# Optimization experiments

Hardware: AMD Instinct MI355X
Metric: run time of the kernel (lower is better)

The kernel has to match this reference:

```python
import jax, jax.numpy as jnp
import numpy as np
from jax import lax

K, INC, OUC = 6, 64, 32
H, W = 512, 512
WIN = 128  # min(128, min(H,W)) for training path
ITERATION = 2  # torch uses random.randint(1,3); fixed for determinism


def setup_inputs() -> dict:
    key = jax.random.key(0)
    ks = jax.random.split(key, 12)
    s = 0.05
    return {
        "x": jax.random.uniform(ks[0], (K, 3, H, W), jnp.float32),
        "pred_list": jax.random.uniform(ks[1], (K, 3, H, W), jnp.float32),
        "feat_list": jax.random.normal(ks[2], (K, INC, H, W), jnp.float32) * 0.1,
        "split_w": jax.random.normal(ks[3], (3 * OUC, INC, 3, 3), jnp.float32) * s,
        "split_b": jax.random.normal(ks[4], (3 * OUC,), jnp.float32) * s,
        "merge1_w": jax.random.normal(ks[5], (INC, 3 * OUC + 3, 3, 3), jnp.float32) * s,
        "merge1_b": jax.random.normal(ks[6], (INC,), jnp.float32) * s,
        "merge2_w": jax.random.normal(ks[7], (INC, INC, 3, 3), jnp.float32) * s,
        "merge2_b": jax.random.normal(ks[8], (INC,), jnp.float32) * s,
        "head_w": jax.random.normal(ks[9], (3, INC, 3, 3), jnp.float32) * s,
        "head_b": jax.random.normal(ks[10], (3,), jnp.float32) * s,
    }


def _conv(x, w, b, groups=1):
    y = lax.conv_general_dilated(
        x, w, (1, 1), ((1, 1), (1, 1)),
        dimension_numbers=("NCHW", "OIHW", "NCHW"), feature_group_count=groups)
    return y + b[None, :, None, None]


def _get_box(pred_list):
    # B_cat = mean of bg channel, T_cat = sum of fg channel; distance map [H,W]
    B_cat = pred_list[:, 2].mean(axis=0)
    T_cat = pred_list[:, 0].sum(axis=0)
    distance = jnp.abs(1.0 - T_cat - B_cat)
    # nearest-neighbor downsample by 0.1: out[i,j] = in[10*i, 10*j]
    hs, ws = H // 10, W // 10
    ds = distance[::10, ::10][:hs, :ws]
    # NMS keep[0] (training path uses boxes[0:1]) == global argmax of score
    idx = jnp.argmax(ds.reshape(-1))
    cx = (idx % ws) * 10
    cy = (idx // ws) * 10
    half = WIN // 2
    x1, y1 = cx - half, cy - half
    x2, y2 = cx + half, cy + half
    ox = (-jnp.minimum(x1, 0) + jnp.minimum(W - x1, 0)
          - jnp.minimum(x2, 0) + jnp.minimum(W - x2, 0))
    oy = (-jnp.minimum(y1, 0) + jnp.minimum(H - y1, 0)
          - jnp.minimum(y2, 0) + jnp.minimum(H - y2, 0))
    return (y1 + oy).astype(jnp.int32), (x1 + ox).astype(jnp.int32)


def reference(x, pred_list, feat_list, split_w, split_b,
              merge1_w, merge1_b, merge2_w, merge2_b, head_w, head_b):
    c = INC
    y1, x1 = _get_box(pred_list)  # box fixed across iterations (computed once)
    x_patch = lax.dynamic_slice(x, (0, 0, y1, x1), (K, 3, WIN, WIN))
    feat_patch = lax.dynamic_slice(feat_list, (0, 0, y1, x1), (K, INC, WIN, WIN))
    feat_tiled = jnp.tile(feat_patch, (1, 3, 1, 1))
    denom = max(K - 1, 1)

    pl = pred_list
    for _ in range(ITERATION):
        pred_patch = lax.dynamic_slice(pl, (0, 0, y1, x1), (K, 3, WIN, WIN))
        # cat([p0.repeat(c), p1.repeat(c), p2.repeat(c)]) == repeat each channel c times
        attention = jnp.repeat(pred_patch, c, axis=1)
        fs = _conv(feat_tiled * attention, split_w, split_b, groups=3)
        f0, f1, f2 = fs[:, :OUC], fs[:, OUC:2 * OUC], fs[:, 2 * OUC:]
        feat_t = f1.sum(0, keepdims=True) / denom - f0.sum(0, keepdims=True) + 2.0 * f0
        feat_r = f0.sum(0, keepdims=True) - f0 + f1
        feat_b = jnp.broadcast_to(f2.mean(0, keepdims=True), f2.shape)
        fcat = jnp.concatenate([feat_t, feat_r, feat_b, x_patch], axis=1)
        h1 = jax.nn.leaky_relu(_conv(fcat, merge1_w, merge1_b), 0.2)
        fm = _conv(h1, merge2_w, merge2_b)
        pr = _conv(fm, head_w, head_b)
        inner = (jnp.tanh(pr[:, :, 10:WIN - 10, 10:WIN - 10]) + 1.0) / 2.0
        pl = lax.dynamic_update_slice(pl, inner, (0, 0, y1 + 10, x1 + 10))
    return pl
```

## Files before the change

### kernel.cpp

```cpp
#include <hip/hip_runtime.h>
#include <math.h>

typedef __attribute__((ext_vector_type(8))) short short8_t;
typedef __attribute__((ext_vector_type(4))) float f32x4;

#define Hh 512
#define Ww 512
#define IMG (Hh * Ww)
#define WINP 128
#define PP (WINP * WINP)

__device__ __forceinline__ unsigned short f2bf(float f) {
    unsigned int u = __builtin_bit_cast(unsigned int, f);
    u += 0x7fffu + ((u >> 16) & 1u);
    return (unsigned short)(u >> 16);
}
__device__ __forceinline__ float bf2f(unsigned short h) {
    unsigned int u = ((unsigned int)h) << 16;
    return __builtin_bit_cast(float, u);
}

__global__ void box_kernel(const float* __restrict__ pred, int* __restrict__ box) {
    int tid = threadIdx.x;
    float best = -1.0f; int bidx = 0x7fffffff;
    for (int cand = tid; cand < 51 * 51; cand += 256) {
        int i = cand / 51, j = cand % 51;
        int y = i * 10, x = j * 10;
        float T = 0.f, Bv = 0.f;
#pragma unroll
        for (int k = 0; k < 6; ++k) {
            T  += pred[((k * 3 + 0) * Hh + y) * Ww + x];
            Bv += pred[((k * 3 + 2) * Hh + y) * Ww + x];
        }
        float d = fabsf(1.0f - T - Bv / 6.0f);
        if (d > best || (d == best && cand < bidx)) { best = d; bidx = cand; }
    }
    __shared__ float sv[256];
    __shared__ int   si[256];
    sv[tid] = best; si[tid] = bidx;
    __syncthreads();
    for (int s = 128; s > 0; s >>= 1) {
        if (tid < s) {
            if (sv[tid + s] > sv[tid] || (sv[tid + s] == sv[tid] && si[tid + s] < si[tid])) {
                sv[tid] = sv[tid + s]; si[tid] = si[tid + s];
            }
        }
        __syncthreads();
    }
    if (tid == 0) {
        int idx = si[0];
        int cy = (idx / 51) * 10, cx = (idx % 51) * 10;
        int yy = cy - 64; yy = yy < 0 ? 0 : (yy > Hh - WINP ? Hh - WINP : yy);
        int xx = cx - 64; xx = xx < 0 ? 0 : (xx > Ww - WINP ? Ww - WINP : xx);
        box[0] = yy; box[1] = xx;
    }
}

__global__ void copy_kernel(const float4* __restrict__ src, float4* __restrict__ dst) {
    int i = blockIdx.x * 256 + threadIdx.x;
    dst[i] = src[i];
}

__global__ void prep_weights(const float* __restrict__ sw, const float* __restrict__ m1w,
                             const float* __restrict__ m2w, const float* __restrict__ hw,
                             unsigned short* __restrict__ WF)
{
    int idx = blockIdx.x * 256 + threadIdx.x;
    int j = idx & 7;
    int lane = (idx >> 3) & 63;
    int frag = idx >> 9;
    int n16 = lane & 15;
    int ko = (lane >> 4) * 8 + j;
    float v = 0.f;
    if (frag < 108) {
        int g = frag / 36; int r = frag % 36; int kc = r / 18; r %= 18; int tap = r / 2; int nf = r & 1;
        int oc = g * 32 + nf * 16 + n16; int ic = kc * 32 + ko;
        v = sw[(oc * 64 + ic) * 9 + tap];
    } else if (frag < 252) {
        int r = frag - 108; int half = r / 72; r %= 72; int kc = r / 18; r %= 18; int tap = r / 2; int nf = r & 1;
        int oc = half * 32 + nf * 16 + n16; int ic = kc * 32 + ko;
        if (ic < 99) v = m1w[(oc * 99 + ic) * 9 + tap];
    } else if (frag < 324) {
        int r = frag - 252; int half = r / 36; r %= 36; int kc = r / 18; r %= 18; int tap = r / 2; int nf = r & 1;
        int oc = half * 32 + nf * 16 + n16; int ic = kc * 32 + ko;
        v = m2w[(oc * 64 + ic) * 9 + tap];
    } else {
        int r = frag - 324; int kc = r / 9; int tap = r % 9;
        int ic = kc * 32 + ko;
        if (n16 < 3) v = hw[(n16 * 64 + ic) * 9 + tap];
    }
    WF[idx] = f2bf(v);
}

__global__ void prep_featcl(const float* __restrict__ feat, const int* __restrict__ box,
                            unsigned short* __restrict__ featcl)
{
    int row = blockIdx.x;
    int k = blockIdx.y;
    int t = threadIdx.x;
    int y1 = box[0], x1 = box[1];
    __shared__ unsigned short s[128 * 64];
    for (int i = 0; i < 32; ++i) {
        int idx = t + i * 256;
        int ic = idx >> 7, c = idx & 127;
        s[c * 64 + ic] = f2bf(feat[((size_t)(k * 64 + ic) * Hh + y1 + row) * Ww + x1 + c]);
    }
    __syncthreads();
    if (t < 128) {
        unsigned short* dst = &featcl[((size_t)k * 16384 + row * 128 + t) * 64];
        for (int i = 0; i < 8; ++i)
            *(short8_t*)&dst[i * 8] = *(short8_t*)&s[t * 64 + i * 8];
    }
}

__global__ __launch_bounds__(256) void split_mfma(
    const unsigned short* __restrict__ featcl, const float* __restrict__ pl,
    const unsigned short* __restrict__ WF, const float* __restrict__ sb,
    const int* __restrict__ box, unsigned short* __restrict__ fscl)
{
    const int tid = threadIdx.x;
    const int l = tid & 63, w = tid >> 6;
    const int T = blockIdx.x;
    const int k = blockIdx.y / 3, g = blockIdx.y % 3;
    const int ty0 = (T >> 3) * 16, tx0 = (T & 7) * 16;
    const int y1 = box[0], x1 = box[1];

    __shared__ __align__(16) unsigned short s_a[10368];
    __shared__ __align__(16) unsigned short s_b[9216];

    f32x4 acc[4][2];
#pragma unroll
    for (int mf = 0; mf < 4; ++mf)
#pragma unroll
        for (int nf = 0; nf < 2; ++nf) acc[mf][nf] = (f32x4){0.f, 0.f, 0.f, 0.f};

    const float* plg = pl + (size_t)(k * 3 + g) * IMG + (size_t)y1 * Ww + x1;
    const unsigned short* fck = featcl + (size_t)k * 16384 * 64;

    for (int kc = 0; kc < 2; ++kc) {
        __syncthreads();
#pragma unroll
        for (int i = 0; i < 6; ++i) {
            int s = tid + i * 256;
            if (s < 1296) {
                int pxs = s >> 2, q = s & 3;
                int r = pxs / 18, c = pxs - r * 18;
                int py = ty0 - 1 + r, px = tx0 - 1 + c;
                short8_t o;
                if (py >= 0 && py < WINP && px >= 0 && px < WINP) {
                    float pv = plg[py * Ww + px];
                    short8_t f = *(const short8_t*)&fck[(size_t)(py * WINP + px) * 64 + kc * 32 + q * 8];
#pragma unroll
                    for (int e = 0; e < 8; ++e) o[e] = (short)f2bf(bf2f((unsigned short)f[e]) * pv);
                } else {
#pragma unroll
                    for (int e = 0; e < 8; ++e) o[e] = 0;
                }
                *(short8_t*)&s_a[(r * 18 + c) * 32 + q * 8] = o;
            }
        }
        {
            const unsigned short* src = WF + (size_t)((g * 2 + kc) * 18) * 512;
#pragma unroll
            for (int i = 0; i < 5; ++i) {
                int cch = tid + i * 256;
                if (cch < 1152)
                    *(short8_t*)&s_b[cch * 8] = *(const short8_t*)&src[cch * 8];
            }
        }
        __syncthreads();
#pragma unroll
        for (int tap = 0; tap < 9; ++tap) {
            int dy = tap / 3, dx = tap % 3;
            short8_t a[4];
#pragma unroll
            for (int mf = 0; mf < 4; ++mf)
                a[mf] = *(const short8_t*)&s_a[((w * 4 + mf + dy) * 18 + (l & 15) + dx) * 32 + (l >> 4) * 8];
#pragma unroll
            for (int nf = 0; nf < 2; ++nf) {
                short8_t bfr = *(const short8_t*)&s_b[((tap * 2 + nf) * 64 + l) * 8];
#pragma unroll
                for (int mf = 0; mf < 4; ++mf)
                    acc[mf][nf] = __builtin_amdgcn_mfma_f32_16x16x32_bf16(a[mf], bfr, acc[mf][nf], 0, 0, 0);
            }
        }
    }
    __syncthreads();
    unsigned short* s_t = s_a;
#pragma unroll
    for (int nf = 0; nf < 2; ++nf) {
        float bias = sb[g * 32 + nf * 16 + (l & 15)];
#pragma unroll
        for (int mf = 0; mf < 4; ++mf) {
            int row = w * 4 + mf;
#pragma unroll
            for (int r = 0; r < 4; ++r) {
                int col = (l >> 4) * 4 + r;
                s_t[(row * 16 + col) * 32 + nf * 16 + (l & 15)] = f2bf(acc[mf][nf][r] + bias);
            }
        }
    }
    __syncthreads();
    {
        int row = tid >> 4, col = tid & 15;
        size_t gpx = (size_t)(ty0 + row) * WINP + tx0 + col;
        unsigned short* dst = fscl + ((size_t)k * 16384 + gpx) * 96 + g * 32;
#pragma unroll
        for (int i = 0; i < 4; ++i)
            *(short8_t*)&dst[i * 8] = *(short8_t*)&s_t[tid * 32 + i * 8];
    }
}

__global__ void reduce_kernel(const unsigned short* __restrict__ fscl, float* __restrict__ Scl)
{
    int tg = blockIdx.x * 256 + threadIdx.x;
    int px = tg >> 2, q = tg & 3;
    float s0[8], s1[8], s2[8];
#pragma unroll
    for (int e = 0; e < 8; ++e) { s0[e] = 0.f; s1[e] = 0.f; s2[e] = 0.f; }
#pragma unroll
    for (int k = 0; k < 6; ++k) {
        const unsigned short* p = &fscl[((size_t)k * 16384 + px) * 96 + q * 8];
        short8_t a0 = *(const short8_t*)&p[0];
        short8_t a1 = *(const short8_t*)&p[32];
        short8_t a2 = *(const short8_t*)&p[64];
#pragma unroll
        for (int e = 0; e < 8; ++e) {
            s0[e] += bf2f((unsigned short)a0[e]);
            s1[e] += bf2f((unsigned short)a1[e]);
            s2[e] += bf2f((unsigned short)a2[e]);
        }
    }
    float* d = &Scl[(size_t)px * 96 + q * 8];
#pragma unroll
    for (int e = 0; e < 8; ++e) {
        d[e]      = s1[e] * 0.2f - s0[e];
        d[32 + e] = s0[e];
        d[64 + e] = s2[e] * (1.f / 6.f);
    }
}

__global__ __launch_bounds__(256) void merge1_mfma(
    const unsigned short* __restrict__ fscl, const float* __restrict__ Scl,
    const float* __restrict__ x, const unsigned short* __restrict__ WF,
    const float* __restrict__ m1b, const int* __restrict__ box,
    unsigned short* __restrict__ h1cl)
{
    const int tid = threadIdx.x;
    const int l = tid & 63, w = tid >> 6;
    const int T = blockIdx.x;
    const int k = blockIdx.y >> 1, half = blockIdx.y & 1;
    const int ty0 = (T >> 3) * 16, tx0 = (T & 7) * 16;
    const int y1 = box[0], x1 = box[1];

    __shared__ __align__(16) unsigned short s_a[10368];
    __shared__ __align__(16) unsigned short s_b[9216];

    f32x4 acc[4][2];
#pragma unroll
    for (int mf = 0; mf < 4; ++mf)
#pragma unroll
        for (int nf = 0; nf < 2; ++nf) acc[mf][nf] = (f32x4){0.f, 0.f, 0.f, 0.f};

    for (int kc = 0; kc < 4; ++kc) {
        __syncthreads();
#pragma unroll
        for (int i = 0; i < 6; ++i) {
            int s = tid + i * 256;
            if (s < 1296) {
                int pxs = s >> 2, q = s & 3;
                int r = pxs / 18, c = pxs - r * 18;
                int py = ty0 - 1 + r, px = tx0 - 1 + c;
                short8_t o;
#pragma unroll
                for (int e = 0; e < 8; ++e) o[e] = 0;
                if (py >= 0 && py < WINP && px >= 0 && px < WINP) {
                    size_t gpx = (size_t)py * WINP + px;
                    if (kc == 0) {
                        short8_t f0 = *(const short8_t*)&fscl[((size_t)k * 16384 + gpx) * 96 + q * 8];
                        const float* S = &Scl[gpx * 96 + q * 8];
#pragma unroll
                        for (int e = 0; e < 8; ++e)
                            o[e] = (short)f2bf(S[e] + 2.f * bf2f((unsigned short)f0[e]));
                    } else if (kc == 1) {
                        const unsigned short* fp = &fscl[((size_t)k * 16384 + gpx) * 96];
                        short8_t f0 = *(const short8_t*)&fp[q * 8];
                        short8_t f1 = *(const short8_t*)&fp[32 + q * 8];
                        const float* S = &Scl[gpx * 96 + 32 + q * 8];
#pragma unroll
                        for (int e = 0; e < 8; ++e)
                            o[e] = (short)f2bf(S[e] - bf2f((unsigned short)f0[e]) + bf2f((unsigned short)f1[e]));
                    } else if (kc == 2) {
                        const float* S = &Scl[gpx * 96 + 64 + q * 8];
#pragma unroll
                        for (int e = 0; e < 8; ++e) o[e] = (short)f2bf(S[e]);
                    } else {
                        if (q == 0) {
#pragma unroll
                            for (int ch = 0; ch < 3; ++ch)
                                o[ch] = (short)f2bf(x[(size_t)(k * 3 + ch) * IMG + (size_t)(y1 + py) * Ww + x1 + px]);
                        }
                    }
                }
                *(short8_t*)&s_a[(r * 18 + c) * 32 + q * 8] = o;
            }
        }
        {
            const unsigned short* src = WF + (size_t)(108 + (half * 4 + kc) * 18) * 512;
#pragma unroll
            for (int i = 0; i < 5; ++i) {
                int cch = tid + i * 256;
                if (cch < 1152)
                    *(short8_t*)&s_b[cch * 8] = *(const short8_t*)&src[cch * 8];
            }
        }
        __syncthreads();
#pragma unroll
        for (int tap = 0; tap < 9; ++tap) {
            int dy = tap / 3, dx = tap % 3;
            short8_t a[4];
#pragma unroll
            for (int mf = 0; mf < 4; ++mf)
                a[mf] = *(const short8_t*)&s_a[((w * 4 + mf + dy) * 18 + (l & 15) + dx) * 32 + (l >> 4) * 8];
#pragma unroll
            for (int nf = 0; nf < 2; ++nf) {
                short8_t bfr = *(const short8_t*)&s_b[((tap * 2 + nf) * 64 + l) * 8];
#pragma unroll
                for (int mf = 0; mf < 4; ++mf)
                    acc[mf][nf] = __builtin_amdgcn_mfma_f32_16x16x32_bf16(a[mf], bfr, acc[mf][nf], 0, 0, 0);
            }
        }
    }
    __syncthreads();
    unsigned short* s_t = s_a;
#pragma unroll
    for (int nf = 0; nf < 2; ++nf) {
        float bias = m1b[half * 32 + nf * 16 + (l & 15)];
#pragma unroll
        for (int mf = 0; mf < 4; ++mf) {
            int row = w * 4 + mf;
#pragma unroll
            for (int r = 0; r < 4; ++r) {
                int col = (l >> 4) * 4 + r;
                float v = acc[mf][nf][r] + bias;
                v = v >= 0.f ? v : 0.2f * v;
                s_t[(row * 16 + col) * 32 + nf * 16 + (l & 15)] = f2bf(v);
            }
        }
    }
    __syncthreads();
    {
        int row = tid >> 4, col = tid & 15;
        size_t gpx = (size_t)(ty0 + row) * WINP + tx0 + col;
        unsigned short* dst = h1cl + ((size_t)k * 16384 + gpx) * 64 + half * 32;
#pragma unroll
        for (int i = 0; i < 4; ++i)
            *(short8_t*)&dst[i * 8] = *(short8_t*)&s_t[tid * 32 + i * 8];
    }
}

__global__ __launch_bounds__(256) void merge2_mfma(
    const unsigned short* __restrict__ h1cl, const unsigned short* __restrict__ WF,
    const float* __restrict__ m2b, unsigned short* __restrict__ h2cl)
{
    const int tid = threadIdx.x;
    const int l = tid & 63, w = tid >> 6;
    const int T = blockIdx.x;
    const int k = blockIdx.y >> 1, half = blockIdx.y & 1;
    const int ty0 = (T >> 3) * 16, tx0 = (T & 7) * 16;

    __shared__ __align__(16) unsigned short s_a[10368];
    __shared__ __align__(16) unsigned short s_b[9216];

    f32x4 acc[4][2];
#pragma unroll
    for (int mf = 0; mf < 4; ++mf)
#pragma unroll
        for (int nf = 0; nf < 2; ++nf) acc[mf][nf] = (f32x4){0.f, 0.f, 0.f, 0.f};

    const unsigned short* ink = h1cl + (size_t)k * 16384 * 64;

    for (int kc = 0; kc < 2; ++kc) {
        __syncthreads();
#pragma unroll
        for (int i = 0; i < 6; ++i) {
            int s = tid + i * 256;
            if (s < 1296) {
                int pxs = s >> 2, q = s & 3;
                int r = pxs / 18, c = pxs - r * 18;
                int py = ty0 - 1 + r, px = tx0 - 1 + c;
                short8_t o;
                if (py >= 0 && py < WINP && px >= 0 && px < WINP) {
                    o = *(const short8_t*)&ink[(size_t)(py * WINP + px) * 64 + kc * 32 + q * 8];
                } else {
#pragma unroll
                    for (int e = 0; e < 8; ++e) o[e] = 0;
                }
                *(short8_t*)&s_a[(r * 18 + c) * 32 + q * 8] = o;
            }
        }
        {
            const unsigned short* src = WF + (size_t)(252 + (half * 2 + kc) * 18) * 512;
#pragma unroll
            for (int i = 0; i < 5; ++i) {
                int cch = tid + i * 256;
                if (cch < 1152)
                    *(short8_t*)&s_b[cch * 8] = *(const short8_t*)&src[cch * 8];
            }
        }
        __syncthreads();
#pragma unroll
        for (int tap = 0; tap < 9; ++tap) {
            int dy = tap / 3, dx = tap % 3;
            short8_t a[4];
#pragma unroll
            for (int mf = 0; mf < 4; ++mf)
                a[mf] = *(const short8_t*)&s_a[((w * 4 + mf + dy) * 18 + (l & 15) + dx) * 32 + (l >> 4) * 8];
#pragma unroll
            for (int nf = 0; nf < 2; ++nf) {
                short8_t bfr = *(const short8_t*)&s_b[((tap * 2 + nf) * 64 + l) * 8];
#pragma unroll
                for (int mf = 0; mf < 4; ++mf)
                    acc[mf][nf] = __builtin_amdgcn_mfma_f32_16x16x32_bf16(a[mf], bfr, acc[mf][nf], 0, 0, 0);
            }
        }
    }
    __syncthreads();
    unsigned short* s_t = s_a;
#pragma unroll
    for (int nf = 0; nf < 2; ++nf) {
        float bias = m2b[half * 32 + nf * 16 + (l & 15)];
#pragma unroll
        for (int mf = 0; mf < 4; ++mf) {
            int row = w * 4 + mf;
#pragma unroll
            for (int r = 0; r < 4; ++r) {
                int col = (l >> 4) * 4 + r;
                s_t[(row * 16 + col) * 32 + nf * 16 + (l & 15)] = f2bf(acc[mf][nf][r] + bias);
            }
        }
    }
    __syncthreads();
    {
        int row = tid >> 4, col = tid & 15;
        size_t gpx = (size_t)(ty0 + row) * WINP + tx0 + col;
        unsigned short* dst = h2cl + ((size_t)k * 16384 + gpx) * 64 + half * 32;
#pragma unroll
        for (int i = 0; i < 4; ++i)
            *(short8_t*)&dst[i * 8] = *(short8_t*)&s_t[tid * 32 + i * 8];
    }
}

__global__ __launch_bounds__(256) void head_mfma(
    const unsigned short* __restrict__ h2cl, const unsigned short* __restrict__ WF,
    const float* __restrict__ hb, const int* __restrict__ box,
    float* __restrict__ out)
{
    const int tid = threadIdx.x;
    const int l = tid & 63, w = tid >> 6;
    const int T = blockIdx.x;
    const int k = blockIdx.y;
    const int oy0 = 10 + (T / 7) * 16, ox0 = 10 + (T % 7) * 16;
    const int y1 = box[0], x1 = box[1];

    __shared__ __align__(16) unsigned short s_a[10368];
    __shared__ __align__(16) unsigned short s_b[4608];

    f32x4 acc[4];
#pragma unroll
    for (int mf = 0; mf < 4; ++mf) acc[mf] = (f32x4){0.f, 0.f, 0.f, 0.f};

    const unsigned short* ink = h2cl + (size_t)k * 16384 * 64;

    for (int kc = 0; kc < 2; ++kc) {
        __syncthreads();
#pragma unroll
        for (int i = 0; i < 6; ++i) {
            int s = tid + i * 256;
            if (s < 1296) {
                int pxs = s >> 2, q = s & 3;
                int r = pxs / 18, c = pxs - r * 18;
                int py = oy0 - 1 + r, px = ox0 - 1 + c;
                *(short8_t*)&s_a[(r * 18 + c) * 32 + q * 8] =
                    *(const short8_t*)&ink[(size_t)(py * WINP + px) * 64 + kc * 32 + q * 8];
            }
        }
        {
            const unsigned short* src = WF + (size_t)(324 + kc * 9) * 512;
#pragma unroll
            for (int i = 0; i < 3; ++i) {
                int cch = tid + i * 256;
                if (cch < 576)
                    *(short8_t*)&s_b[cch * 8] = *(const short8_t*)&src[cch * 8];
            }
        }
        __syncthreads();
#pragma unroll
        for (int tap = 0; tap < 9; ++tap) {
            int dy = tap / 3, dx = tap % 3;
            short8_t bfr = *(const short8_t*)&s_b[(tap * 64 + l) * 8];
#pragma unroll
            for (int mf = 0; mf < 4; ++mf) {
                short8_t a = *(const short8_t*)&s_a[((w * 4 + mf + dy) * 18 + (l & 15) + dx) * 32 + (l >> 4) * 8];
                acc[mf] = __builtin_amdgcn_mfma_f32_16x16x32_bf16(a, bfr, acc[mf], 0, 0, 0);
            }
        }
    }
    int oc = l & 15;
    if (oc < 3) {
        float bias = hb[oc];
#pragma unroll
        for (int mf = 0; mf < 4; ++mf) {
            int row = oy0 + w * 4 + mf;
            if (row < 118) {
#pragma unroll
                for (int r = 0; r < 4; ++r) {
                    int col = ox0 + (l >> 4) * 4 + r;
                    if (col < 118) {
                        float v = (tanhf(acc[mf][r] + bias) + 1.0f) * 0.5f;
                        out[(size_t)(k * 3 + oc) * IMG + (size_t)(y1 + row) * Ww + x1 + col] = v;
                    }
                }
            }
        }
    }
}

extern "C" void kernel_launch(void* const* d_in, const int* in_sizes, int n_in,
                              void* d_out, int out_size, void* d_ws, size_t ws_size,
                              hipStream_t stream)
{
    const float* x       = (const float*)d_in[0];
    const float* pred    = (const float*)d_in[1];
    const float* feat    = (const float*)d_in[2];
    const float* split_w = (const float*)d_in[3];
    const float* split_b = (const float*)d_in[4];
    const float* m1w     = (const float*)d_in[5];
    const float* m1b     = (const float*)d_in[6];
    const float* m2w     = (const float*)d_in[7];
    const float* m2b     = (const float*)d_in[8];
    const float* hw      = (const float*)d_in[9];
    const float* hb      = (const float*)d_in[10];
    float* out = (float*)d_out;

    char* base = (char*)d_ws;
    size_t o = 0;
    int* box = (int*)(base + o);                  o += 256;
    unsigned short* WF = (unsigned short*)(base + o);      o += (size_t)175104 * 2;  o = (o + 255) & ~(size_t)255;
    unsigned short* featcl = (unsigned short*)(base + o);  o += (size_t)6 * 16384 * 64 * 2;
    unsigned short* fscl = (unsigned short*)(base + o);    o += (size_t)6 * 16384 * 96 * 2;
    float* Scl = (float*)(base + o);                       o += (size_t)16384 * 96 * 4;
    unsigned short* h1cl = (unsigned short*)(base + o);    o += (size_t)6 * 16384 * 64 * 2;
    unsigned short* h2cl = (unsigned short*)(base + o);    o += (size_t)6 * 16384 * 64 * 2;

    box_kernel<<<1, 256, 0, stream>>>(pred, box);
    prep_weights<<<684, 256, 0, stream>>>(split_w, m1w, m2w, hw, WF);
    prep_featcl<<<dim3(128, 6), 256, 0, stream>>>(feat, box, featcl);
    copy_kernel<<<4608, 256, 0, stream>>>((const float4*)pred, (float4*)out);

    for (int it = 0; it < 2; ++it) {
        split_mfma<<<dim3(64, 18), 256, 0, stream>>>(featcl, out, WF, split_b, box, fscl);
        reduce_kernel<<<256, 256, 0, stream>>>(fscl, Scl);
        merge1_mfma<<<dim3(64, 12), 256, 0, stream>>>(fscl, Scl, x, WF, m1b, box, h1cl);
        merge2_mfma<<<dim3(64, 12), 256, 0, stream>>>(h1cl, WF, m2b, h2cl);
        head_mfma<<<dim3(49, 6), 256, 0, stream>>>(h2cl, WF, hb, box, out);
    }
}
```

Before: 698.8 us.

## Fuse prep kernels, precompute modulated split input, fuse merge2 with head

Merges weight packing, output copy and feature modulation into one prep launch, and writes pre-multiplied bf16 attention-modulated features per plane so the split conv only loads tiles. The reduce step and the fcat construction move into a combine kernel, so merge1 reads a ready channel-last buffer. merge2 and head are fused into one kernel that recomputes a haloed h2 tile in shared memory, dropping the h2 round trip through global memory. Split and merge1 now use 512-thread blocks with taller tiles and padded LDS strides. The costs are halo recomputation, more LDS per block and an extra modulate pass between iterations.

New measurement: 756.9 us. +8.3%, slower.

```diff
diff --git a/kernel.cpp b/kernel.cpp
--- a/kernel.cpp
+++ b/kernel.cpp
@@ -8,7 +8,9 @@
 #define Ww 512
 #define IMG (Hh * Ww)
 #define WINP 128
-#define PP (WINP * WINP)
+#define NPX 16384
+#define AST 40
+#define H1ST 72
 
 __device__ __forceinline__ unsigned short f2bf(float f) {
     unsigned int u = __builtin_bit_cast(unsigned int, f);
@@ -56,16 +58,10 @@
     }
 }
 
-__global__ void copy_kernel(const float4* __restrict__ src, float4* __restrict__ dst) {
-    int i = blockIdx.x * 256 + threadIdx.x;
-    dst[i] = src[i];
-}
-
-__global__ void prep_weights(const float* __restrict__ sw, const float* __restrict__ m1w,
-                             const float* __restrict__ m2w, const float* __restrict__ hw,
-                             unsigned short* __restrict__ WF)
-{
-    int idx = blockIdx.x * 256 + threadIdx.x;
+__device__ __forceinline__ void weights_body(int idx, const float* sw, const float* m1w,
+                                             const float* m2w, const float* hw,
+                                             unsigned short* WF)
+{
     int j = idx & 7;
     int lane = (idx >> 3) & 63;
     int frag = idx >> 9;
@@ -92,41 +88,63 @@
     WF[idx] = f2bf(v);
 }
 
-__global__ void prep_featcl(const float* __restrict__ feat, const int* __restrict__ box,
-                            unsigned short* __restrict__ featcl)
-{
-    int row = blockIdx.x;
-    int k = blockIdx.y;
-    int t = threadIdx.x;
+__device__ __forceinline__ void modulate_body(int idx, const float* feat, const float* pl,
+                                              const int* box, unsigned short* msplit)
+{
+    int q = idx & 7;
+    int px = (idx >> 3) & (NPX - 1);
+    int plane = idx >> 17;
+    int k = plane / 3, g = plane % 3;
     int y1 = box[0], x1 = box[1];
-    __shared__ unsigned short s[128 * 64];
-    for (int i = 0; i < 32; ++i) {
-        int idx = t + i * 256;
-        int ic = idx >> 7, c = idx & 127;
-        s[c * 64 + ic] = f2bf(feat[((size_t)(k * 64 + ic) * Hh + y1 + row) * Ww + x1 + c]);
-    }
-    __syncthreads();
-    if (t < 128) {
-        unsigned short* dst = &featcl[((size_t)k * 16384 + row * 128 + t) * 64];
-        for (int i = 0; i < 8; ++i)
-            *(short8_t*)&dst[i * 8] = *(short8_t*)&s[t * 64 + i * 8];
-    }
-}
-
-__global__ __launch_bounds__(256) void split_mfma(
-    const unsigned short* __restrict__ featcl, const float* __restrict__ pl,
-    const unsigned short* __restrict__ WF, const float* __restrict__ sb,
-    const int* __restrict__ box, unsigned short* __restrict__ fscl)
+    int py = px >> 7, pxc = px & 127;
+    size_t goff = (size_t)(y1 + py) * Ww + x1 + pxc;
+    float pv = pl[(size_t)(k * 3 + g) * IMG + goff];
+    const float* fb = feat + (size_t)k * 64 * IMG + goff;
+    short8_t o;
+#pragma unroll
+    for (int e = 0; e < 8; ++e)
+        o[e] = (short)f2bf(fb[(size_t)(q * 8 + e) * IMG] * pv);
+    int kc = q >> 2, ql = q & 3;
+    *(short8_t*)&msplit[((size_t)(plane * 2 + kc) * NPX + px) * 32 + ql * 8] = o;
+}
+
+__global__ void modulate_kernel(const float* __restrict__ feat, const float* __restrict__ pl,
+                                const int* __restrict__ box, unsigned short* __restrict__ msplit)
+{
+    modulate_body(blockIdx.x * 256 + threadIdx.x, feat, pl, box, msplit);
+}
+
+__global__ void prep_all(const float* __restrict__ sw, const float* __restrict__ m1w,
+                         const float* __restrict__ m2w, const float* __restrict__ hw,
+                         unsigned short* __restrict__ WF,
+                         const float4* __restrict__ pred4, float4* __restrict__ out4,
+                         const float* __restrict__ feat, const float* __restrict__ pred,
+                         const int* __restrict__ box, unsigned short* __restrict__ msplit)
+{
+    int b = blockIdx.x, t = threadIdx.x;
+    if (b < 684) {
+        weights_body(b * 256 + t, sw, m1w, m2w, hw, WF);
+    } else if (b < 5292) {
+        int i = (b - 684) * 256 + t;
+        out4[i] = pred4[i];
+    } else {
+        modulate_body((b - 5292) * 256 + t, feat, pred, box, msplit);
+    }
+}
+
+__global__ __launch_bounds__(512, 4) void split_mfma(
+    const unsigned short* __restrict__ msplit, const unsigned short* __restrict__ WF,
+    const float* __restrict__ sb, unsigned short* __restrict__ fscl)
 {
     const int tid = threadIdx.x;
     const int l = tid & 63, w = tid >> 6;
     const int T = blockIdx.x;
-    const int k = blockIdx.y / 3, g = blockIdx.y % 3;
-    const int ty0 = (T >> 3) * 16, tx0 = (T & 7) * 16;
-    const int y1 = box[0], x1 = box[1];
-
-    __shared__ __align__(16) unsigned short s_a[10368];
-    __shared__ __align__(16) unsigned short s_b[9216];
+    const int plane = blockIdx.y;
+    const int k = plane / 3, g = plane % 3;
+    const int ty0 = (T >> 3) * 32, tx0 = (T & 7) * 16;
+
+    __shared__ __align__(16) unsigned short s_a[612 * AST];
+    __shared__ __align__(16) unsigned short s_b[18 * 512];
 
     f32x4 acc[4][2];
 #pragma unroll
@@ -134,54 +152,44 @@
 #pragma unroll
         for (int nf = 0; nf < 2; ++nf) acc[mf][nf] = (f32x4){0.f, 0.f, 0.f, 0.f};
 
-    const float* plg = pl + (size_t)(k * 3 + g) * IMG + (size_t)y1 * Ww + x1;
-    const unsigned short* fck = featcl + (size_t)k * 16384 * 64;
+    const int colb = l & 15, qo = (l >> 4) * 8;
 
     for (int kc = 0; kc < 2; ++kc) {
         __syncthreads();
-#pragma unroll
-        for (int i = 0; i < 6; ++i) {
-            int s = tid + i * 256;
-            if (s < 1296) {
-                int pxs = s >> 2, q = s & 3;
-                int r = pxs / 18, c = pxs - r * 18;
-                int py = ty0 - 1 + r, px = tx0 - 1 + c;
-                short8_t o;
-                if (py >= 0 && py < WINP && px >= 0 && px < WINP) {
-                    float pv = plg[py * Ww + px];
-                    short8_t f = *(const short8_t*)&fck[(size_t)(py * WINP + px) * 64 + kc * 32 + q * 8];
-#pragma unroll
-                    for (int e = 0; e < 8; ++e) o[e] = (short)f2bf(bf2f((unsigned short)f[e]) * pv);
-                } else {
-#pragma unroll
-                    for (int e = 0; e < 8; ++e) o[e] = 0;
-                }
-                *(short8_t*)&s_a[(r * 18 + c) * 32 + q * 8] = o;
-            }
+        const unsigned short* msp = msplit + (size_t)(plane * 2 + kc) * NPX * 32;
+        for (int u = tid; u < 2448; u += 512) {
+            int pxs = u >> 2, q = u & 3;
+            int r = pxs / 18, c = pxs - r * 18;
+            int py = ty0 - 1 + r, px = tx0 - 1 + c;
+            short8_t o;
+            if (py >= 0 && py < WINP && px >= 0 && px < WINP) {
+                o = *(const short8_t*)&msp[(size_t)(py * WINP + px) * 32 + q * 8];
+            } else {
+#pragma unroll
+                for (int e = 0; e < 8; ++e) o[e] = 0;
+            }
+            *(short8_t*)&s_a[pxs * AST + q * 8] = o;
         }
         {
             const unsigned short* src = WF + (size_t)((g * 2 + kc) * 18) * 512;
-#pragma unroll
-            for (int i = 0; i < 5; ++i) {
-                int cch = tid + i * 256;
-                if (cch < 1152)
-                    *(short8_t*)&s_b[cch * 8] = *(const short8_t*)&src[cch * 8];
-            }
-        }
-        __syncthreads();
-#pragma unroll
-        for (int tap = 0; tap < 9; ++tap) {
-            int dy = tap / 3, dx = tap % 3;
-            short8_t a[4];
-#pragma unroll
-            for (int mf = 0; mf < 4; ++mf)
-                a[mf] = *(const short8_t*)&s_a[((w * 4 + mf + dy) * 18 + (l & 15) + dx) * 32 + (l >> 4) * 8];
+            for (int u = tid; u < 1152; u += 512)
+                *(short8_t*)&s_b[u * 8] = *(const short8_t*)&src[u * 8];
+        }
+        __syncthreads();
+#pragma unroll
+        for (int dx = 0; dx < 3; ++dx) {
+            short8_t a6[6];
+#pragma unroll
+            for (int i = 0; i < 6; ++i)
+                a6[i] = *(const short8_t*)&s_a[((w * 4 + i) * 18 + colb + dx) * AST + qo];
+#pragma unroll
+            for (int dy = 0; dy < 3; ++dy)
 #pragma unroll
             for (int nf = 0; nf < 2; ++nf) {
-                short8_t bfr = *(const short8_t*)&s_b[((tap * 2 + nf) * 64 + l) * 8];
+                short8_t b = *(const short8_t*)&s_b[(((dy * 3 + dx) * 2 + nf) * 64 + l) * 8];
 #pragma unroll
                 for (int mf = 0; mf < 4; ++mf)
-                    acc[mf][nf] = __builtin_amdgcn_mfma_f32_16x16x32_bf16(a[mf], bfr, acc[mf][nf], 0, 0, 0);
+                    acc[mf][nf] = __builtin_amdgcn_mfma_f32_16x16x32_bf16(a6[mf + dy], b, acc[mf][nf], 0, 0, 0);
             }
         }
     }
@@ -195,8 +203,8 @@
             int row = w * 4 + mf;
 #pragma unroll
             for (int r = 0; r < 4; ++r) {
-                int col = (l >> 4) * 4 + r;
-                s_t[(row * 16 + col) * 32 + nf * 16 + (l & 15)] = f2bf(acc[mf][nf][r] + bias);
+                int colpx = (l >> 4) * 4 + r;
+                s_t[(row * 16 + colpx) * 32 + nf * 16 + (l & 15)] = f2bf(acc[mf][nf][r] + bias);
             }
         }
     }
@@ -204,57 +212,98 @@
     {
         int row = tid >> 4, col = tid & 15;
         size_t gpx = (size_t)(ty0 + row) * WINP + tx0 + col;
-        unsigned short* dst = fscl + ((size_t)k * 16384 + gpx) * 96 + g * 32;
+        unsigned short* dst = fscl + ((size_t)k * NPX + gpx) * 96 + g * 32;
 #pragma unroll
         for (int i = 0; i < 4; ++i)
             *(short8_t*)&dst[i * 8] = *(short8_t*)&s_t[tid * 32 + i * 8];
     }
 }
 
-__global__ void reduce_kernel(const unsigned short* __restrict__ fscl, float* __restrict__ Scl)
-{
-    int tg = blockIdx.x * 256 + threadIdx.x;
-    int px = tg >> 2, q = tg & 3;
-    float s0[8], s1[8], s2[8];
-#pragma unroll
-    for (int e = 0; e < 8; ++e) { s0[e] = 0.f; s1[e] = 0.f; s2[e] = 0.f; }
-#pragma unroll
-    for (int k = 0; k < 6; ++k) {
-        const unsigned short* p = &fscl[((size_t)k * 16384 + px) * 96 + q * 8];
-        short8_t a0 = *(const short8_t*)&p[0];
-        short8_t a1 = *(const short8_t*)&p[32];
-        short8_t a2 = *(const short8_t*)&p[64];
+__global__ void combine_kernel(const unsigned short* __restrict__ fscl,
+                               const float* __restrict__ x, const int* __restrict__ box,
+                               unsigned short* __restrict__ fcat)
+{
+    const int tid = threadIdx.x;
+    const int px0 = blockIdx.x * 64;
+    const int y1 = box[0], x1 = box[1];
+    __shared__ float s_S[64 * 96];
+
+    {
+        int px_l = tid >> 2, q = tid & 3;
+        int px = px0 + px_l;
+        float s0[8], s1[8], s2[8];
+#pragma unroll
+        for (int e = 0; e < 8; ++e) { s0[e] = 0.f; s1[e] = 0.f; s2[e] = 0.f; }
+#pragma unroll
+        for (int k = 0; k < 6; ++k) {
+            const unsigned short* p = &fscl[((size_t)k * NPX + px) * 96 + q * 8];
+            short8_t a0 = *(const short8_t*)&p[0];
+            short8_t a1 = *(const short8_t*)&p[32];
+            short8_t a2 = *(const short8_t*)&p[64];
+#pragma unroll
+            for (int e = 0; e < 8; ++e) {
+                s0[e] += bf2f((unsigned short)a0[e]);
+                s1[e] += bf2f((unsigned short)a1[e]);
+                s2[e] += bf2f((unsigned short)a2[e]);
+            }
+        }
 #pragma unroll
         for (int e = 0; e < 8; ++e) {
-            s0[e] += bf2f((unsigned short)a0[e]);
-            s1[e] += bf2f((unsigned short)a1[e]);
-            s2[e] += bf2f((unsigned short)a2[e]);
-        }
-    }
-    float* d = &Scl[(size_t)px * 96 + q * 8];
-#pragma unroll
-    for (int e = 0; e < 8; ++e) {
-        d[e]      = s1[e] * 0.2f - s0[e];
-        d[32 + e] = s0[e];
-        d[64 + e] = s2[e] * (1.f / 6.f);
-    }
-}
-
-__global__ __launch_bounds__(256) void merge1_mfma(
-    const unsigned short* __restrict__ fscl, const float* __restrict__ Scl,
-    const float* __restrict__ x, const unsigned short* __restrict__ WF,
-    const float* __restrict__ m1b, const int* __restrict__ box,
-    unsigned short* __restrict__ h1cl)
+            s_S[px_l * 96 + q * 8 + e]      = s1[e] * 0.2f - s0[e];
+            s_S[px_l * 96 + 32 + q * 8 + e] = s0[e];
+            s_S[px_l * 96 + 64 + q * 8 + e] = s2[e] * (1.f / 6.f);
+        }
+    }
+    __syncthreads();
+    for (int u = tid; u < 384; u += 256) {
+        int k = u >> 6, px_l = u & 63;
+        int px = px0 + px_l;
+        int py = px >> 7, pxc = px & 127;
+        const unsigned short* fp = &fscl[((size_t)k * NPX + px) * 96];
+#pragma unroll
+        for (int q = 0; q < 4; ++q) {
+            short8_t f0 = *(const short8_t*)&fp[q * 8];
+            short8_t f1 = *(const short8_t*)&fp[32 + q * 8];
+            short8_t o0, o1, o2;
+#pragma unroll
+            for (int e = 0; e < 8; ++e) {
+                float v0 = bf2f((unsigned short)f0[e]);
+                float v1 = bf2f((unsigned short)f1[e]);
+                o0[e] = (short)f2bf(s_S[px_l * 96 + q * 8 + e] + 2.f * v0);
+                o1[e] = (short)f2bf(s_S[px_l * 96 + 32 + q * 8 + e] - v0 + v1);
+                o2[e] = (short)f2bf(s_S[px_l * 96 + 64 + q * 8 + e]);
+            }
+            *(short8_t*)&fcat[((size_t)(0 * 6 + k) * NPX + px) * 32 + q * 8] = o0;
+            *(short8_t*)&fcat[((size_t)(1 * 6 + k) * NPX + px) * 32 + q * 8] = o1;
+            *(short8_t*)&fcat[((size_t)(2 * 6 + k) * NPX + px) * 32 + q * 8] = o2;
+        }
+        short8_t xz;
+#pragma unroll
+        for (int e = 0; e < 8; ++e) xz[e] = 0;
+#pragma unroll
+        for (int ch = 0; ch < 3; ++ch)
+            xz[ch] = (short)f2bf(x[(size_t)(k * 3 + ch) * IMG + (size_t)(y1 + py) * Ww + x1 + pxc]);
+        unsigned short* d3 = &fcat[((size_t)(3 * 6 + k) * NPX + px) * 32];
+        *(short8_t*)&d3[0] = xz;
+        short8_t z;
+#pragma unroll
+        for (int e = 0; e < 8; ++e) z[e] = 0;
+        *(short8_t*)&d3[8] = z; *(short8_t*)&d3[16] = z; *(short8_t*)&d3[24] = z;
+    }
+}
+
+__global__ __launch_bounds__(512, 4) void merge1_mfma(
+    const unsigned short* __restrict__ fcat, const unsigned short* __restrict__ WF,
+    const float* __restrict__ m1b, unsigned short* __restrict__ h1cl)
 {
     const int tid = threadIdx.x;
     const int l = tid & 63, w = tid >> 6;
     const int T = blockIdx.x;
     const int k = blockIdx.y >> 1, half = blockIdx.y & 1;
-    const int ty0 = (T >> 3) * 16, tx0 = (T & 7) * 16;
-    const int y1 = box[0], x1 = box[1];
-
-    __shared__ __align__(16) unsigned short s_a[10368];
-    __shared__ __align__(16) unsigned short s_b[9216];
+    const int ty0 = (T >> 3) * 32, tx0 = (T & 7) * 16;
+
+    __shared__ __align__(16) unsigned short s_a[612 * AST];
+    __shared__ __align__(16) unsigned short s_b[18 * 512];
 
     f32x4 acc[4][2];
 #pragma unroll
@@ -262,72 +311,44 @@
 #pragma unroll
         for (int nf = 0; nf < 2; ++nf) acc[mf][nf] = (f32x4){0.f, 0.f, 0.f, 0.f};
 
+    const int colb = l & 15, qo = (l >> 4) * 8;
+
     for (int kc = 0; kc < 4; ++kc) {
         __syncthreads();
-#pragma unroll
-        for (int i = 0; i < 6; ++i) {
-            int s = tid + i * 256;
-            if (s < 1296) {
-                int pxs = s >> 2, q = s & 3;
-                int r = pxs / 18, c = pxs - r * 18;
-                int py = ty0 - 1 + r, px = tx0 - 1 + c;
-                short8_t o;
+        const unsigned short* src_a = fcat + (size_t)(kc * 6 + k) * NPX * 32;
+        for (int u = tid; u < 2448; u += 512) {
+            int pxs = u >> 2, q = u & 3;
+            int r = pxs / 18, c = pxs - r * 18;
+            int py = ty0 - 1 + r, px = tx0 - 1 + c;
+            short8_t o;
+            if (py >= 0 && py < WINP && px >= 0 && px < WINP) {
+                o = *(const short8_t*)&src_a[(size_t)(py * WINP + px) * 32 + q * 8];
+            } else {
 #pragma unroll
                 for (int e = 0; e < 8; ++e) o[e] = 0;
-                if (py >= 0 && py < WINP && px >= 0 && px < WINP) {
-                    size_t gpx = (size_t)py * WINP + px;
-                    if (kc == 0) {
-                        short8_t f0 = *(const short8_t*)&fscl[((size_t)k * 16384 + gpx) * 96 + q * 8];
-                        const float* S = &Scl[gpx * 96 + q * 8];
-#pragma unroll
-                        for (int e = 0; e < 8; ++e)
-                            o[e] = (short)f2bf(S[e] + 2.f * bf2f((unsigned short)f0[e]));
-                    } else if (kc == 1) {
-                        const unsigned short* fp = &fscl[((size_t)k * 16384 + gpx) * 96];
-                        short8_t f0 = *(const short8_t*)&fp[q * 8];
-                        short8_t f1 = *(const short8_t*)&fp[32 + q * 8];
-                        const float* S = &Scl[gpx * 96 + 32 + q * 8];
-#pragma unroll
-                        for (int e = 0; e < 8; ++e)
-                            o[e] = (short)f2bf(S[e] - bf2f((unsigned short)f0[e]) + bf2f((unsigned short)f1[e]));
-                    } else if (kc == 2) {
-                        const float* S = &Scl[gpx * 96 + 64 + q * 8];
-#pragma unroll
-                        for (int e = 0; e < 8; ++e) o[e] = (short)f2bf(S[e]);
-                    } else {
-                        if (q == 0) {
-#pragma unroll
-                            for (int ch = 0; ch < 3; ++ch)
-                                o[ch] = (short)f2bf(x[(size_t)(k * 3 + ch) * IMG + (size_t)(y1 + py) * Ww + x1 + px]);
-                        }
-                    }
-                }
-                *(short8_t*)&s_a[(r * 18 + c) * 32 + q * 8] = o;
-            }
+            }
+            *(short8_t*)&s_a[pxs * AST + q * 8] = o;
         }
         {
-            const unsigned short* src = WF + (size_t)(108 + (half * 4 + kc) * 18) * 512;
-#pragma unroll
-            for (int i = 0; i < 5; ++i) {
-                int cch = tid + i * 256;
-                if (cch < 1152)
-                    *(short8_t*)&s_b[cch * 8] = *(const short8_t*)&src[cch * 8];
-            }
-        }
-        __syncthreads();
-#pragma unroll
-        for (int tap = 0; tap < 9; ++tap) {
-            int dy = tap / 3, dx = tap % 3;
-            short8_t a[4];
-#pragma unroll
-            for (int mf = 0; mf < 4; ++mf)
-                a[mf] = *(const short8_t*)&s_a[((w * 4 + mf + dy) * 18 + (l & 15) + dx) * 32 + (l >> 4) * 8];
+            const unsigned short* src = WF + (size_t)((108 + (half * 4 + kc) * 18)) * 512;
+            for (int u = tid; u < 1152; u += 512)
+                *(short8_t*)&s_b[u * 8] = *(const short8_t*)&src[u * 8];
+        }
+        __syncthreads();
+#pragma unroll
+        for (int dx = 0; dx < 3; ++dx) {
+            short8_t a6[6];
+#pragma unroll
+            for (int i = 0; i < 6; ++i)
+                a6[i] = *(const short8_t*)&s_a[((w * 4 + i) * 18 + colb + dx) * AST + qo];
+#pragma unroll
+            for (int dy = 0; dy < 3; ++dy)
 #pragma unroll
             for (int nf = 0; nf < 2; ++nf) {
-                short8_t bfr = *(const short8_t*)&s_b[((tap * 2 + nf) * 64 + l) * 8];
+                short8_t b = *(const short8_t*)&s_b[(((dy * 3 + dx) * 2 + nf) * 64 + l) * 8];
 #pragma unroll
                 for (int mf = 0; mf < 4; ++mf)
-                    acc[mf][nf] = __builtin_amdgcn_mfma_f32_16x16x32_bf16(a[mf], bfr, acc[mf][nf], 0, 0, 0);
+                    acc[mf][nf] = __builtin_amdgcn_mfma_f32_16x16x32_bf16(a6[mf + dy], b, acc[mf][nf], 0, 0, 0);
             }
         }
     }
@@ -341,10 +362,10 @@
             int row = w * 4 + mf;
 #pragma unroll
             for (int r = 0; r < 4; ++r) {
-                int col = (l >> 4) * 4 + r;
+                int colpx = (l >> 4) * 4 + r;
                 float v = acc[mf][nf][r] + bias;
                 v = v >= 0.f ? v : 0.2f * v;
-                s_t[(row * 16 + col) * 32 + nf * 16 + (l & 15)] = f2bf(v);
+                s_t[(row * 16 + colpx) * 32 + nf * 16 + (l & 15)] = f2bf(v);
             }
         }
     }
@@ -352,109 +373,17 @@
     {
         int row = tid >> 4, col = tid & 15;
         size_t gpx = (size_t)(ty0 + row) * WINP + tx0 + col;
-        unsigned short* dst = h1cl + ((size_t)k * 16384 + gpx) * 64 + half * 32;
+        unsigned short* dst = h1cl + ((size_t)k * NPX + gpx) * 64 + half * 32;
 #pragma unroll
         for (int i = 0; i < 4; ++i)
             *(short8_t*)&dst[i * 8] = *(short8_t*)&s_t[tid * 32 + i * 8];
     }
 }
 
-__global__ __launch_bounds__(256) void merge2_mfma(
+__global__ __launch_bounds__(256, 1) void mergehead(
     const unsigned short* __restrict__ h1cl, const unsigned short* __restrict__ WF,
-    const float* __restrict__ m2b, unsigned short* __restrict__ h2cl)
-{
-    const int tid = threadIdx.x;
-    const int l = tid & 63, w = tid >> 6;
-    const int T = blockIdx.x;
-    const int k = blockIdx.y >> 1, half = blockIdx.y & 1;
-    const int ty0 = (T >> 3) * 16, tx0 = (T & 7) * 16;
-
-    __shared__ __align__(16) unsigned short s_a[10368];
-    __shared__ __align__(16) unsigned short s_b[9216];
-
-    f32x4 acc[4][2];
-#pragma unroll
-    for (int mf = 0; mf < 4; ++mf)
-#pragma unroll
-        for (int nf = 0; nf < 2; ++nf) acc[mf][nf] = (f32x4){0.f, 0.f, 0.f, 0.f};
-
-    const unsigned short* ink = h1cl + (size_t)k * 16384 * 64;
-
-    for (int kc = 0; kc < 2; ++kc) {
-        __syncthreads();
-#pragma unroll
-        for (int i = 0; i < 6; ++i) {
-            int s = tid + i * 256;
-            if (s < 1296) {
-                int pxs = s >> 2, q = s & 3;
-                int r = pxs / 18, c = pxs - r * 18;
-                int py = ty0 - 1 + r, px = tx0 - 1 + c;
-                short8_t o;
-                if (py >= 0 && py < WINP && px >= 0 && px < WINP) {
-                    o = *(const short8_t*)&ink[(size_t)(py * WINP + px) * 64 + kc * 32 + q * 8];
-                } else {
-#pragma unroll
-                    for (int e = 0; e < 8; ++e) o[e] = 0;
-                }
-                *(short8_t*)&s_a[(r * 18 + c) * 32 + q * 8] = o;
-            }
-        }
-        {
-            const unsigned short* src = WF + (size_t)(252 + (half * 2 + kc) * 18) * 512;
-#pragma unroll
-            for (int i = 0; i < 5; ++i) {
-                int cch = tid + i * 256;
-                if (cch < 1152)
-                    *(short8_t*)&s_b[cch * 8] = *(const short8_t*)&src[cch * 8];
-            }
-        }
-        __syncthreads();
-#pragma unroll
-        for (int tap = 0; tap < 9; ++tap) {
-            int dy = tap / 3, dx = tap % 3;
-            short8_t a[4];
-#pragma unroll
-            for (int mf = 0; mf < 4; ++mf)
-                a[mf] = *(const short8_t*)&s_a[((w * 4 + mf + dy) * 18 + (l & 15) + dx) * 32 + (l >> 4) * 8];
-#pragma unroll
-            for (int nf = 0; nf < 2; ++nf) {
-                short8_t bfr = *(const short8_t*)&s_b[((tap * 2 + nf) * 64 + l) * 8];
-#pragma unroll
-                for (int mf = 0; mf < 4; ++mf)
-                    acc[mf][nf] = __builtin_amdgcn_mfma_f32_16x16x32_bf16(a[mf], bfr, acc[mf][nf], 0, 0, 0);
-            }
-        }
-    }
-    __syncthreads();
-    unsigned short* s_t = s_a;
-#pragma unroll
-    for (int nf = 0; nf < 2; ++nf) {
-        float bias = m2b[half * 32 + nf * 16 + (l & 15)];
-#pragma unroll
-        for (int mf = 0; mf < 4; ++mf) {
-            int row = w * 4 + mf;
-#pragma unroll
-            for (int r = 0; r < 4; ++r) {
-                int col = (l >> 4) * 4 + r;
-                s_t[(row * 16 + col) * 32 + nf * 16 + (l & 15)] = f2bf(acc[mf][nf][r] + bias);
-            }
-        }
-    }
-    __syncthreads();
-    {
-        int row = tid >> 4, col = tid & 15;
-        size_t gpx = (size_t)(ty0 + row) * WINP + tx0 + col;
-        unsigned short* dst = h2cl + ((size_t)k * 16384 + gpx) * 64 + half * 32;
-#pragma unroll
-        for (int i = 0; i < 4; ++i)
-            *(short8_t*)&dst[i * 8] = *(short8_t*)&s_t[tid * 32 + i * 8];
-    }
-}
-
-__global__ __launch_bounds__(256) void head_mfma(
-    const unsigned short* __restrict__ h2cl, const unsigned short* __restrict__ WF,
-    const float* __restrict__ hb, const int* __restrict__ box,
-    float* __restrict__ out)
+    const float* __restrict__ m2b, const float* __restrict__ hb,
+    const int* __restrict__ box, float* __restrict__ out)
 {
     const int tid = threadIdx.x;
     const int l = tid & 63, w = tid >> 6;
@@ -463,47 +392,92 @@
     const int oy0 = 10 + (T / 7) * 16, ox0 = 10 + (T % 7) * 16;
     const int y1 = box[0], x1 = box[1];
 
-    __shared__ __align__(16) unsigned short s_a[10368];
-    __shared__ __align__(16) unsigned short s_b[4608];
-
-    f32x4 acc[4];
-#pragma unroll
-    for (int mf = 0; mf < 4; ++mf) acc[mf] = (f32x4){0.f, 0.f, 0.f, 0.f};
-
-    const unsigned short* ink = h2cl + (size_t)k * 16384 * 64;
-
+    __shared__ __align__(16) unsigned short s_h1[400 * H1ST];
+    __shared__ __align__(16) unsigned short s_h2[324 * H1ST];
+    __shared__ __align__(16) unsigned short s_b[36 * 512];
+
+    {
+        const unsigned short* src = h1cl + (size_t)k * NPX * 64;
+        for (int u = tid; u < 3200; u += 256) {
+            int pxs = u >> 3, q = u & 7;
+            int r = pxs / 20, c = pxs - r * 20;
+            int py = oy0 - 2 + r, px = ox0 - 2 + c;
+            *(short8_t*)&s_h1[pxs * H1ST + q * 8] =
+                *(const short8_t*)&src[(size_t)(py * WINP + px) * 64 + q * 8];
+        }
+    }
+
+    int rr[6], cc[6];
+#pragma unroll
+    for (int mf = 0; mf < 6; ++mf) {
+        int pxb = (mf * 4 + w) * 16 + (l & 15);
+        int px = pxb < 324 ? pxb : 0;
+        rr[mf] = px / 18; cc[mf] = px - rr[mf] * 18;
+    }
+    f32x4 acc[6][4];
+#pragma unroll
+    for (int mf = 0; mf < 6; ++mf)
+#pragma unroll
+        for (int nf = 0; nf < 4; ++nf) acc[mf][nf] = (f32x4){0.f, 0.f, 0.f, 0.f};
+
+    const int qo = (l >> 4) * 8;
     for (int kc = 0; kc < 2; ++kc) {
         __syncthreads();
-#pragma unroll
-        for (int i = 0; i < 6; ++i) {
-            int s = tid + i * 256;
-            if (s < 1296) {
-                int pxs = s >> 2, q = s & 3;
-                int r = pxs / 18, c = pxs - r * 18;
-                int py = oy0 - 1 + r, px = ox0 - 1 + c;
-                *(short8_t*)&s_a[(r * 18 + c) * 32 + q * 8] =
-                    *(const short8_t*)&ink[(size_t)(py * WINP + px) * 64 + kc * 32 + q * 8];
-            }
-        }
-        {
-            const unsigned short* src = WF + (size_t)(324 + kc * 9) * 512;
-#pragma unroll
-            for (int i = 0; i < 3; ++i) {
-                int cch = tid + i * 256;
-                if (cch < 576)
-                    *(short8_t*)&s_b[cch * 8] = *(const short8_t*)&src[cch * 8];
-            }
+        for (int u = tid; u < 2304; u += 256) {
+            int f = u >> 6, within = u & 63;
+            int tap = f >> 2, nf = f & 3;
+            int srcfrag = 252 + ((nf >> 1) * 2 + kc) * 18 + tap * 2 + (nf & 1);
+            *(short8_t*)&s_b[(size_t)f * 512 + within * 8] =
+                *(const short8_t*)&WF[(size_t)srcfrag * 512 + within * 8];
         }
         __syncthreads();
 #pragma unroll
         for (int tap = 0; tap < 9; ++tap) {
             int dy = tap / 3, dx = tap % 3;
-            short8_t bfr = *(const short8_t*)&s_b[(tap * 64 + l) * 8];
-#pragma unroll
-            for (int mf = 0; mf < 4; ++mf) {
-                short8_t a = *(const short8_t*)&s_a[((w * 4 + mf + dy) * 18 + (l & 15) + dx) * 32 + (l >> 4) * 8];
-                acc[mf] = __builtin_amdgcn_mfma_f32_16x16x32_bf16(a, bfr, acc[mf], 0, 0, 0);
-            }
+            short8_t a[6];
+#pragma unroll
+            for (int mf = 0; mf < 6; ++mf)
+                a[mf] = *(const short8_t*)&s_h1[((rr[mf] + dy) * 20 + cc[mf] + dx) * H1ST + kc * 32 + qo];
+#pragma unroll
+            for (int nf = 0; nf < 4; ++nf) {
+                short8_t b = *(const short8_t*)&s_b[((tap * 4 + nf) * 64 + l) * 8];
+#pragma unroll
+                for (int mf = 0; mf < 6; ++mf)
+                    acc[mf][nf] = __builtin_amdgcn_mfma_f32_16x16x32_bf16(a[mf], b, acc[mf][nf], 0, 0, 0);
+            }
+        }
+    }
+    __syncthreads();
+#pragma unroll
+    for (int nf = 0; nf < 4; ++nf) {
+        float bias = m2b[nf * 16 + (l & 15)];
+#pragma unroll
+        for (int mf = 0; mf < 6; ++mf) {
+#pragma unroll
+            for (int r = 0; r < 4; ++r) {
+                int px = (mf * 4 + w) * 16 + (l >> 4) * 4 + r;
+                if (px < 324)
+                    s_h2[px * H1ST + nf * 16 + (l & 15)] = f2bf(acc[mf][nf][r] + bias);
+            }
+        }
+    }
+    for (int u = tid; u < 1152; u += 256)
+        *(short8_t*)&s_b[u * 8] = *(const short8_t*)&WF[(size_t)324 * 512 + u * 8];
+    __syncthreads();
+
+    f32x4 acc2[4];
+#pragma unroll
+    for (int mf = 0; mf < 4; ++mf) acc2[mf] = (f32x4){0.f, 0.f, 0.f, 0.f};
+#pragma unroll
+    for (int kc = 0; kc < 2; ++kc)
+#pragma unroll
+    for (int tap = 0; tap < 9; ++tap) {
+        int dy = tap / 3, dx = tap % 3;
+        short8_t b = *(const short8_t*)&s_b[((kc * 9 + tap) * 64 + l) * 8];
+#pragma unroll
+        for (int mf = 0; mf < 4; ++mf) {
+            short8_t a = *(const short8_t*)&s_h2[((w * 4 + mf + dy) * 18 + (l & 15) + dx) * H1ST + kc * 32 + qo];
+            acc2[mf] = __builtin_amdgcn_mfma_f32_16x16x32_bf16(a, b, acc2[mf], 0, 0, 0);
         }
     }
     int oc = l & 15;
@@ -511,14 +485,14 @@
         float bias = hb[oc];
 #pragma unroll
         for (int mf = 0; mf < 4; ++mf) {
-            int row = oy0 + w * 4 + mf;
-            if (row < 118) {
+            int orow = oy0 + w * 4 + mf;
+            if (orow < 118) {
 #pragma unroll
                 for (int r = 0; r < 4; ++r) {
-                    int col = ox0 + (l >> 4) * 4 + r;
-                    if (col < 118) {
-                        float v = (tanhf(acc[mf][r] + bias) + 1.0f) * 0.5f;
-                        out[(size_t)(k * 3 + oc) * IMG + (size_t)(y1 + row) * Ww + x1 + col] = v;
+                    int ocol = ox0 + (l >> 4) * 4 + r;
+                    if (ocol < 118) {
+                        float v = (tanhf(acc2[mf][r] + bias) + 1.0f) * 0.5f;
+                        out[(size_t)(k * 3 + oc) * IMG + (size_t)(y1 + orow) * Ww + x1 + ocol] = v;
                     }
                 }
             }
@@ -545,24 +519,24 @@
 
     char* base = (char*)d_ws;
     size_t o = 0;
-    int* box = (int*)(base + o);                  o += 256;
+    int* box = (int*)(base + o);                           o += 256;
     unsigned short* WF = (unsigned short*)(base + o);      o += (size_t)175104 * 2;  o = (o + 255) & ~(size_t)255;
-    unsigned short* featcl = (unsigned short*)(base + o);  o += (size_t)6 * 16384 * 64 * 2;
-    unsigned short* fscl = (unsigned short*)(base + o);    o += (size_t)6 * 16384 * 96 * 2;
-    float* Scl = (float*)(base + o);                       o += (size_t)16384 * 96 * 4;
-    unsigned short* h1cl = (unsigned short*)(base + o);    o += (size_t)6 * 16384 * 64 * 2;
-    unsigned short* h2cl = (unsigned short*)(base + o);    o += (size_t)6 * 16384 * 64 * 2;
+    unsigned short* msplit = (unsigned short*)(base + o);  o += (size_t)36 * NPX * 32 * 2;
+    unsigned short* fscl = (unsigned short*)(base + o);    o += (size_t)6 * NPX * 96 * 2;
+    unsigned short* fcat = (unsigned short*)(base + o);    o += (size_t)24 * NPX * 32 * 2;
+    unsigned short* h1cl = (unsigned short*)(base + o);    o += (size_t)6 * NPX * 64 * 2;
 
     box_kernel<<<1, 256, 0, stream>>>(pred, box);
-    prep_weights<<<684, 256, 0, stream>>>(split_w, m1w, m2w, hw, WF);
-    prep_featcl<<<dim3(128, 6), 256, 0, stream>>>(feat, box, featcl);
-    copy_kernel<<<4608, 256, 0, stream>>>((const float4*)pred, (float4*)out);
+    prep_all<<<14508, 256, 0, stream>>>(split_w, m1w, m2w, hw, WF,
+                                        (const float4*)pred, (float4*)out,
+                                        feat, pred, box, msplit);
 
     for (int it = 0; it < 2; ++it) {
-        split_mfma<<<dim3(64, 18), 256, 0, stream>>>(featcl, out, WF, split_b, box, fscl);
-        reduce_kernel<<<256, 256, 0, stream>>>(fscl, Scl);
-        merge1_mfma<<<dim3(64, 12), 256, 0, stream>>>(fscl, Scl, x, WF, m1b, box, h1cl);
-        merge2_mfma<<<dim3(64, 12), 256, 0, stream>>>(h1cl, WF, m2b, h2cl);
-        head_mfma<<<dim3(49, 6), 256, 0, stream>>>(h2cl, WF, hb, box, out);
-    }
-}
+        split_mfma<<<dim3(32, 18), 512, 0, stream>>>(msplit, WF, split_b, fscl);
+        combine_kernel<<<256, 256, 0, stream>>>(fscl, x, box, fcat);
+        merge1_mfma<<<dim3(32, 12), 512, 0, stream>>>(fcat, WF, m1b, h1cl);
+        mergehead<<<dim3(49, 6), 256, 0, stream>>>(h1cl, WF, m2b, hb, box, out);
+        if (it == 0)
+            modulate_kernel<<<9216, 256, 0, stream>>>(feat, out, box, msplit);
+    }
+}
```
